# Kernel tuning notes

Measured on AMD Instinct MI355X. Metric: run time of the kernel, lower is better.

The kernel has to match this reference:

```python
import jax, jax.numpy as jnp
import numpy as np

DIM = 512
DEPTH = 6
HEADS = 8
DH = 64
WS = 256
INNER = HEADS * DH  # 512
FF_INNER = int(DIM * 4 * 2 / 3)  # 1365
QK_SCALE = 8.0


def l2norm(x):
    n = jnp.linalg.norm(x, axis=-1, keepdims=True)
    return x / jnp.maximum(n, 1e-12)


def rotate_half(x):
    x1, x2 = jnp.split(x, 2, axis=-1)
    return jnp.concatenate([-x2, x1], axis=-1)


def apply_xpos_rotary(q, k, n, dh, scale_base):
    # SinusoidalEmbeddings with use_xpos=True, scale_base = window_size // 2
    inv_freq = 1.0 / (10000.0 ** (jnp.arange(0, dh, 2, dtype=jnp.float32) / dh))  # (dh/2,)
    t = jnp.arange(n, dtype=jnp.float32)
    freqs = t[:, None] * inv_freq[None, :]                     # (n, dh/2)
    freqs = jnp.concatenate([freqs, freqs], axis=-1)           # (n, dh)
    sv = (jnp.arange(0, dh, 2, dtype=jnp.float32) + 0.4 * dh) / (1.4 * dh)  # (dh/2,)
    power = (t - n // 2) / scale_base
    xs = sv[None, :] ** power[:, None]                         # (n, dh/2)
    xs = jnp.concatenate([xs, xs], axis=-1)                    # (n, dh)
    cos, sin = jnp.cos(freqs), jnp.sin(freqs)
    q = q * cos * xs + rotate_half(q) * sin * xs
    k = k * cos / xs + rotate_half(k) * sin / xs
    return q, k


def local_mha(x, Wqkv, Wo, q_scale, k_scale):
    b, n, d = x.shape
    qkv = x @ Wqkv                                             # (b, n, 3*INNER)
    q, k, v = jnp.split(qkv, 3, axis=-1)
    to_heads = lambda t: t.reshape(b, n, HEADS, DH).transpose(0, 2, 1, 3)
    q, k, v = to_heads(q), to_heads(k), to_heads(v)            # (b, h, n, dh)
    # qk rmsnorm (l2 norm + learned per-dim scale), fixed attn scale = 8
    q = l2norm(q) * q_scale
    k = l2norm(k) * k_scale
    q, k = apply_xpos_rotary(q, k, n, DH, WS // 2)
    w = n // WS
    bucket = lambda t: t.reshape(b, HEADS, w, WS, DH)
    bq, bk, bv = bucket(q), bucket(k), bucket(v)
    # look_around: prepend previous window (look_backward=1, look_forward=0)
    def look_around(t):
        prev = jnp.concatenate([jnp.zeros_like(t[:, :, :1]), t[:, :, :-1]], axis=2)
        return jnp.concatenate([prev, t], axis=3)              # (b, h, w, 2*WS, dh)
    bk2, bv2 = look_around(bk), look_around(bv)
    # positions and masks (causal + exact windowsize + pad)
    tq = jnp.arange(n, dtype=jnp.int32).reshape(w, WS)
    tk_prev = jnp.concatenate([jnp.full((1, WS), -1, dtype=jnp.int32), tq[:-1]], axis=0)
    tk = jnp.concatenate([tk_prev, tq], axis=1)                # (w, 2*WS)
    diff = tq[:, :, None] - tk[:, None, :]
    allowed = (diff >= 0) & (diff <= WS) & (tk[:, None, :] >= 0)  # (w, WS, 2*WS)
    sim = jnp.einsum('bhwie,bhwje->bhwij', bq, bk2) * QK_SCALE
    sim = jnp.where(allowed, sim, -jnp.finfo(sim.dtype).max)
    attn = jax.nn.softmax(sim, axis=-1)
    o = jnp.einsum('bhwij,bhwje->bhwie', attn, bv2)            # (b, h, w, WS, dh)
    o = o.reshape(b, HEADS, n, DH).transpose(0, 2, 1, 3).reshape(b, n, INNER)
    return o @ Wo


def feedforward(x, W1, b1, W2, b2):
    h = x @ W1 + b1
    a, g = jnp.split(h, 2, axis=-1)
    return (a * jax.nn.gelu(g, approximate=False)) @ W2 + b2


def setup_inputs() -> dict:
    key = jax.random.key(0)
    ks = jax.random.split(key, 8)
    s = 0.02
    x = jax.random.normal(ks[0], (1, 8192, DIM), dtype=jnp.float32)
    Wqkv = jax.random.normal(ks[1], (DEPTH, DIM, 3 * INNER), dtype=jnp.float32) * s
    Wo = jax.random.normal(ks[2], (DEPTH, INNER, DIM), dtype=jnp.float32) * s
    q_scale = jnp.ones((DEPTH, DH), dtype=jnp.float32)
    k_scale = jnp.ones((DEPTH, DH), dtype=jnp.float32)
    W1 = jax.random.normal(ks[3], (DEPTH, DIM, 2 * FF_INNER), dtype=jnp.float32) * s
    b1 = jnp.zeros((DEPTH, 2 * FF_INNER), dtype=jnp.float32)
    W2 = jax.random.normal(ks[4], (DEPTH, FF_INNER, DIM), dtype=jnp.float32) * s
    b2 = jnp.zeros((DEPTH, DIM), dtype=jnp.float32)
    return {"x": x, "Wqkv": Wqkv, "Wo": Wo, "q_scale": q_scale, "k_scale": k_scale,
            "W1": W1, "b1": b1, "W2": W2, "b2": b2}


def reference(x, Wqkv, Wo, q_scale, k_scale, W1, b1, W2, b2):
    for i in range(DEPTH):
        x = local_mha(x, Wqkv[i], Wo[i], q_scale[i], k_scale[i]) + x
        x = feedforward(x, W1[i], b1[i], W2[i], b2[i]) + x
    return x
```

## Files before the change

### kernel.cpp

```cpp
#include <hip/hip_runtime.h>
#include <hip/hip_bf16.h>
#include <math.h>

typedef short s16x8 __attribute__((ext_vector_type(8)));
typedef short s16x4 __attribute__((ext_vector_type(4)));
typedef float f32x4 __attribute__((ext_vector_type(4)));

#define MFMA(A,B,C) __builtin_amdgcn_mfma_f32_16x16x32_bf16((A),(B),(C),0,0,0)

typedef __attribute__((address_space(3))) unsigned int lds_u32;
typedef __attribute__((address_space(1))) const unsigned int glb_u32;
__device__ __forceinline__ void gload16(const short* g, const short* l){
  __builtin_amdgcn_global_load_lds((glb_u32*)g, (lds_u32*)l, 16, 0, 0);
}

__device__ __forceinline__ float bf2f(short u){
  unsigned int x = ((unsigned int)(unsigned short)u) << 16;
  return __builtin_bit_cast(float, x);
}
__device__ __forceinline__ short f2bf(float f){
  unsigned int x = __builtin_bit_cast(unsigned int, f);
  x += 0x7fffu + ((x >> 16) & 1u);
  return (short)(x >> 16);
}
__device__ __forceinline__ float gelu_t(float x){
  float u = x + 0.044715f*x*x*x;
  float e = __expf(1.5957691216057308f*u);
  float th = 1.f - 2.f/(e + 1.f);
  return 0.5f*x*(1.f + th);
}

__device__ __forceinline__ void xcd_swz(int gx, int gy, int &bx, int &by){
  int id = bx + by*gx;
  int nwg = gx*gy;
  int q = nwg >> 3, r = nwg & 7;
  int xcd = id & 7, idx = id >> 3;
  int nid = (xcd < r ? xcd*(q+1) : r*(q+1) + (xcd-r)*q) + idx;
  bx = nid % gx; by = nid / gx;
}

#define FFI 1365
#define FFIP 1376

template<int HAS_BIAS, int HAS_RES, int OUT_F32, int OUT_BF16>
__global__ __launch_bounds__(512) void gemm_k(
    const short* __restrict__ A, const short* __restrict__ Bt,
    const float* __restrict__ bias, const float* __restrict__ res,
    float* __restrict__ outF, short* __restrict__ outB,
    int M, int N, int K)
{
  __shared__ short As[2][128*32];
  __shared__ short Bs[2][128*32];
  const int tid = threadIdx.x;
  const int lane = tid & 63, wv = tid >> 6;
  const int g = lane >> 4, qi = lane & 15;
  int bx = blockIdx.x, by = blockIdx.y;
  xcd_swz(gridDim.x, gridDim.y, bx, by);
  const int m0 = bx * 128, n0 = by * 128;
  const int wm = (wv >> 2) * 64, wn = (wv & 3) * 32;

  const int sr = tid >> 2, sc = (tid & 3) * 8;
  const short* Ag = A  + (size_t)(m0 + sr)*K + sc;
  const short* Bg = Bt + (size_t)(n0 + sr)*K + sc;

  f32x4 acc[4][2];
  #pragma unroll
  for (int i=0;i<4;i++)
    #pragma unroll
    for (int j=0;j<2;j++) acc[i][j] = (f32x4){0.f,0.f,0.f,0.f};

  auto stage = [&](int buf, int k0){
    gload16(Ag + k0, &As[buf][wv*512]);
    gload16(Bg + k0, &Bs[buf][wv*512]);
  };

  const int nt = K >> 5;
  stage(0, 0);
  __syncthreads();
  for (int t = 0; t < nt; ++t) {
    const int cur = t & 1;
    if (t + 1 < nt) stage(cur ^ 1, (t+1) << 5);
    s16x8 af[4], bf[2];
    #pragma unroll
    for (int mi=0;mi<4;mi++) af[mi] = *(const s16x8*)&As[cur][(wm+mi*16+qi)*32 + g*8];
    #pragma unroll
    for (int ni=0;ni<2;ni++) bf[ni] = *(const s16x8*)&Bs[cur][(wn+ni*16+qi)*32 + g*8];
    #pragma unroll
    for (int mi=0;mi<4;mi++)
      #pragma unroll
      for (int ni=0;ni<2;ni++)
        acc[mi][ni] = MFMA(af[mi], bf[ni], acc[mi][ni]);
    __syncthreads();
  }
  #pragma unroll
  for (int mi=0;mi<4;mi++){
    #pragma unroll
    for (int r=0;r<4;r++){
      int row = m0 + wm + mi*16 + g*4 + r;
      #pragma unroll
      for (int ni=0;ni<2;ni++){
        int col = n0 + wn + ni*16 + qi;
        float v = acc[mi][ni][r];
        if (HAS_BIAS) v += bias[col];
        if (HAS_RES)  v += res[(size_t)row*N + col];
        if (OUT_F32)  outF[(size_t)row*N + col] = v;
        if (OUT_BF16) outB[(size_t)row*N + col] = f2bf(v);
      }
    }
  }
}

template<int HAS_BIAS, int HAS_RES, int OUT_F32, int OUT_BF16>
__global__ __launch_bounds__(256) void gemm64_k(
    const short* __restrict__ A, const short* __restrict__ Bt,
    const float* __restrict__ bias, const float* __restrict__ res,
    float* __restrict__ outF, short* __restrict__ outB,
    int M, int N, int K)
{
  __shared__ short As[2][64*32];
  __shared__ short Bs[2][64*32];
  const int tid = threadIdx.x;
  const int lane = tid & 63, wv = tid >> 6;
  const int g = lane >> 4, qi = lane & 15;
  int bx = blockIdx.x, by = blockIdx.y;
  xcd_swz(gridDim.x, gridDim.y, bx, by);
  const int m0 = bx * 64, n0 = by * 64;
  const int wm = (wv >> 1) * 32, wn = (wv & 1) * 32;

  const int sr = tid >> 2, sc = (tid & 3) * 8;
  const short* Ag = A  + (size_t)(m0 + sr)*K + sc;
  const short* Bg = Bt + (size_t)(n0 + sr)*K + sc;

  f32x4 acc[2][2];
  #pragma unroll
  for (int i=0;i<2;i++)
    #pragma unroll
    for (int j=0;j<2;j++) acc[i][j] = (f32x4){0.f,0.f,0.f,0.f};

  auto stage = [&](int buf, int k0){
    gload16(Ag + k0, &As[buf][wv*512]);
    gload16(Bg + k0, &Bs[buf][wv*512]);
  };

  const int nt = K >> 5;
  stage(0, 0);
  __syncthreads();
  for (int t = 0; t < nt; ++t) {
    const int cur = t & 1;
    if (t + 1 < nt) stage(cur ^ 1, (t+1) << 5);
    s16x8 af[2], bf[2];
    #pragma unroll
    for (int mi=0;mi<2;mi++) af[mi] = *(const s16x8*)&As[cur][(wm+mi*16+qi)*32 + g*8];
    #pragma unroll
    for (int ni=0;ni<2;ni++) bf[ni] = *(const s16x8*)&Bs[cur][(wn+ni*16+qi)*32 + g*8];
    #pragma unroll
    for (int mi=0;mi<2;mi++)
      #pragma unroll
      for (int ni=0;ni<2;ni++)
        acc[mi][ni] = MFMA(af[mi], bf[ni], acc[mi][ni]);
    __syncthreads();
  }
  #pragma unroll
  for (int mi=0;mi<2;mi++){
    #pragma unroll
    for (int r=0;r<4;r++){
      int row = m0 + wm + mi*16 + g*4 + r;
      #pragma unroll
      for (int ni=0;ni<2;ni++){
        int col = n0 + wn + ni*16 + qi;
        float v = acc[mi][ni][r];
        if (HAS_BIAS) v += bias[col];
        if (HAS_RES)  v += res[(size_t)row*N + col];
        if (OUT_F32)  outF[(size_t)row*N + col] = v;
        if (OUT_BF16) outB[(size_t)row*N + col] = f2bf(v);
      }
    }
  }
}

__global__ __launch_bounds__(512) void geglu_k(
    const short* __restrict__ A, const short* __restrict__ Bt,
    const float* __restrict__ b1, short* __restrict__ hg)
{
  __shared__ short As[2][128*32];
  __shared__ short Ba[2][128*32];
  __shared__ short Bg[2][128*32];
  const int tid = threadIdx.x;
  const int lane = tid & 63, wv = tid >> 6;
  const int g = lane >> 4, qi = lane & 15;
  int bx = blockIdx.x, by = blockIdx.y;
  xcd_swz(gridDim.x, gridDim.y, bx, by);
  const int m0 = bx * 128, n0 = by * 128;
  const int wm = (wv >> 2) * 64, wn = (wv & 3) * 32;

  const int sr = tid >> 2, sc = (tid & 3) * 8;
  const short* Ag = A + (size_t)(m0 + sr)*512 + sc;
  const short* Pa = Bt + (size_t)min(n0 + sr, FFI-1)*512 + sc;
  const short* Pg = Bt + (size_t)min(FFI + n0 + sr, 2729)*512 + sc;

  f32x4 aa[4][2], ag[4][2];
  #pragma unroll
  for (int i=0;i<4;i++)
    #pragma unroll
    for (int j=0;j<2;j++){ aa[i][j]=(f32x4){0.f,0.f,0.f,0.f}; ag[i][j]=(f32x4){0.f,0.f,0.f,0.f}; }

  auto stage = [&](int buf, int k0){
    gload16(Ag + k0, &As[buf][wv*512]);
    gload16(Pa + k0, &Ba[buf][wv*512]);
    gload16(Pg + k0, &Bg[buf][wv*512]);
  };

  stage(0, 0);
  __syncthreads();
  for (int t = 0; t < 16; ++t) {
    const int cur = t & 1;
    if (t + 1 < 16) stage(cur ^ 1, (t+1) << 5);
    s16x8 af[4], bfa[2], bfg[2];
    #pragma unroll
    for (int mi=0;mi<4;mi++) af[mi] = *(const s16x8*)&As[cur][(wm+mi*16+qi)*32 + g*8];
    #pragma unroll
    for (int ni=0;ni<2;ni++){ bfa[ni] = *(const s16x8*)&Ba[cur][(wn+ni*16+qi)*32 + g*8];
                              bfg[ni] = *(const s16x8*)&Bg[cur][(wn+ni*16+qi)*32 + g*8]; }
    #pragma unroll
    for (int mi=0;mi<4;mi++)
      #pragma unroll
      for (int ni=0;ni<2;ni++){
        aa[mi][ni] = MFMA(af[mi], bfa[ni], aa[mi][ni]);
        ag[mi][ni] = MFMA(af[mi], bfg[ni], ag[mi][ni]);
      }
    __syncthreads();
  }
  #pragma unroll
  for (int mi=0;mi<4;mi++){
    #pragma unroll
    for (int r=0;r<4;r++){
      int row = m0 + wm + mi*16 + g*4 + r;
      #pragma unroll
      for (int ni=0;ni<2;ni++){
        int col = n0 + wn + ni*16 + qi;
        if (col < FFI){
          float va = aa[mi][ni][r] + b1[col];
          float vg = ag[mi][ni][r] + b1[FFI+col];
          hg[(size_t)row*FFIP + col] = f2bf(va * gelu_t(vg));
        } else if (col < FFIP){
          hg[(size_t)row*FFIP + col] = 0;
        }
      }
    }
  }
}

__global__ void rope_k(float* __restrict__ tab){
  int n = blockIdx.x, dd = threadIdx.x;
  int i = dd & 31;
  double invf = pow(10000.0, -(double)i/32.0);
  double fr = (double)n * invf;
  double c = cos(fr), s = sin(fr);
  double sv = (2.0*i + 25.6)/89.6;
  double pw = ((double)n - 4096.0)/128.0;
  double xs = pow(sv, pw);
  size_t o = (size_t)n*64 + dd;
  tab[o]            = (float)(c*xs);
  tab[524288+o]     = (float)(s*xs);
  tab[2*524288+o]   = (float)(c/xs);
  tab[3*524288+o]   = (float)(s/xs);
}

__global__ __launch_bounds__(256) void wtrans_k(
    const float* __restrict__ src, short* __restrict__ dst,
    int K, int N, int Kp, long srcStride, long dstStride)
{
  __shared__ float t[64][65];
  const float* s = src + (size_t)blockIdx.z * srcStride;
  short* d = dst + (size_t)blockIdx.z * dstStride;
  int n0 = blockIdx.x*64, k0 = blockIdx.y*64;
  int tid = threadIdx.x;
  #pragma unroll
  for (int p=0;p<4;p++){
    int task = p*256+tid;
    int r = task>>4, c = (task&15)*4;
    int k = k0 + r;
    #pragma unroll
    for (int e=0;e<4;e++){
      int n = n0+c+e;
      t[r][c+e] = (k<K && n<N) ? s[(size_t)k*N+n] : 0.f;
    }
  }
  __syncthreads();
  #pragma unroll
  for (int p=0;p<2;p++){
    int task = p*256+tid;
    int nr = task>>3, kg=(task&7)*8;
    int n = n0+nr;
    if (n < N && (k0+kg) < Kp){
      s16x8 v;
      #pragma unroll
      for (int j=0;j<8;j++) v[j] = f2bf(t[kg+j][nr]);
      *(s16x8*)(d + (size_t)n*Kp + k0 + kg) = v;
    }
  }
}

__global__ void cast_k(const float* __restrict__ in, short* __restrict__ out){
  int i = (blockIdx.x*256+threadIdx.x)*4;
  float4 v = *(const float4*)(in+i);
  s16x4 o = { f2bf(v.x), f2bf(v.y), f2bf(v.z), f2bf(v.w) };
  *(s16x4*)(out+i) = o;
}

__global__ __launch_bounds__(256) void qkprep_k(
    const short* __restrict__ qkv, const float* __restrict__ tab,
    const float* __restrict__ qs, const float* __restrict__ ks,
    short* __restrict__ qrot, short* __restrict__ krot)
{
  int wv = threadIdx.x >> 6, lane = threadIdx.x & 63;
  float qsc = qs[lane], ksc = ks[lane];
  #pragma unroll
  for (int it=0; it<8; ++it){
    int wid = it*8192 + blockIdx.x*4 + wv;
    int n = wid >> 3, h = wid & 7;
    float qv = bf2f(qkv[(size_t)n*1536 + h*64 + lane]);
    float kv = bf2f(qkv[(size_t)n*1536 + 512 + h*64 + lane]);
    float sq = qv*qv, sk = kv*kv;
    #pragma unroll
    for (int m=1;m<64;m<<=1){ sq += __shfl_xor(sq,m,64); sk += __shfl_xor(sk,m,64); }
    qv *= qsc / fmaxf(sqrtf(sq), 1e-12f);
    kv *= ksc / fmaxf(sqrtf(sk), 1e-12f);
    float qo = __shfl_xor(qv,32,64), ko = __shfl_xor(kv,32,64);
    float sgn = (lane<32)? -1.f : 1.f;
    size_t to = (size_t)n*64 + lane;
    float cq = tab[to], sxq = tab[524288+to], ck = tab[2*524288+to], sxk = tab[3*524288+to];
    qrot[((size_t)h*8192+n)*64+lane] = f2bf(qv*cq + sgn*qo*sxq);
    krot[((size_t)h*8192+n)*64+lane] = f2bf(kv*ck + sgn*ko*sxk);
  }
}

__global__ __launch_bounds__(256) void vtrans_k(const short* __restrict__ qkv, short* __restrict__ vt){
  __shared__ short t[64][72];
  int n0 = blockIdx.x*64, h = blockIdx.y;
  int tid = threadIdx.x;
  #pragma unroll
  for (int p=0;p<2;p++){
    int task = p*256+tid;
    int r = task>>3, cg = (task&7)*8;
    *(s16x8*)&t[r][cg] = *(const s16x8*)(qkv + (size_t)(n0+r)*1536 + 1024 + h*64 + cg);
  }
  __syncthreads();
  #pragma unroll
  for (int p=0;p<2;p++){
    int task = p*256+tid;
    int d = task>>3, nb = (task&7)*8;
    s16x8 v;
    #pragma unroll
    for (int j=0;j<8;j++) v[j] = t[nb+j][d];
    *(s16x8*)(vt + ((size_t)h*64+d)*8192 + n0 + nb) = v;
  }
}

__global__ __launch_bounds__(512,1) void attn_k(
    const short* __restrict__ qrot, const short* __restrict__ krot,
    const short* __restrict__ vt, short* __restrict__ attn_o)
{
  __shared__ short Ks[128][72];
  __shared__ short Vs[64][136];
  const int bxx = blockIdx.x, h = blockIdx.y;
  const int w = bxx >> 1, half = bxx & 1;
  const int tid = threadIdx.x, lane = tid & 63, wv = tid >> 6;
  const int g = lane >> 4, qi = lane & 15;
  const int wq = half*128 + wv*16;
  const int q0abs = w*256 + wq;
  s16x8 qf[2];
  {
    const short* p = qrot + ((size_t)h*8192 + q0abs + qi)*64 + g*8;
    qf[0] = *(const s16x8*)p;
    qf[1] = *(const s16x8*)(p + 32);
  }
  f32x4 oacc[4];
  #pragma unroll
  for (int j=0;j<4;j++) oacc[j]=(f32x4){0.f,0.f,0.f,0.f};
  float mrun = -1e30f, lrun = 0.f;
  const int kvbase = w*256 - 256;
  for (int s=half; s<half+3; ++s){
    __syncthreads();
    #pragma unroll
    for (int p=0;p<2;p++){
      int task = p*512 + tid;
      {
        int r = task>>3, cg = (task&7)*8;
        int jg = kvbase + s*128 + r;
        s16x8 v = {0,0,0,0,0,0,0,0};
        if (jg>=0) v = *(const s16x8*)(krot + ((size_t)h*8192+jg)*64 + cg);
        *(s16x8*)&Ks[r][cg] = v;
      }
      {
        int dd = task>>4, cg = (task&15)*8;
        int jg = kvbase + s*128 + cg;
        s16x8 v = {0,0,0,0,0,0,0,0};
        if (jg>=0) v = *(const s16x8*)(vt + ((size_t)h*64+dd)*8192 + jg);
        *(s16x8*)&Vs[dd][cg] = v;
      }
    }
    __syncthreads();
    for (int cc=0;cc<2;cc++){
      const int jlo = s*128 + cc*64;
      if (jlo + 63 < wq) continue;
      if (jlo > wq + 271) continue;
      if (w==0 && jlo < 256) continue;
      f32x4 sacc[4];
      #pragma unroll
      for (int i=0;i<4;i++) sacc[i]=(f32x4){0.f,0.f,0.f,0.f};
      #pragma unroll
      for (int ks=0;ks<2;ks++){
        s16x8 kf[4];
        #pragma unroll
        for (int mi=0;mi<4;mi++) kf[mi] = *(const s16x8*)&Ks[cc*64+mi*16+qi][ks*32+g*8];
        #pragma unroll
        for (int mi=0;mi<4;mi++)
          sacc[mi] = MFMA(kf[mi], qf[ks], sacc[mi]);
      }
      const bool interior = (jlo >= wq+15) && (jlo+63 <= wq+256);
      float cmax = -1e30f;
      #pragma unroll
      for (int mi=0;mi<4;mi++)
        #pragma unroll
        for (int r=0;r<4;r++){
          float x = sacc[mi][r] * 8.f;
          if (!interior){
            int j = jlo + mi*16 + g*4 + r;
            int ql = wq + qi;
            if (j < ql || j > ql+256) x = -1e30f;
          }
          sacc[mi][r] = x;
          cmax = fmaxf(cmax, x);
        }
      cmax = fmaxf(cmax, __shfl_xor(cmax,16,64));
      cmax = fmaxf(cmax, __shfl_xor(cmax,32,64));
      float mn = fmaxf(mrun, cmax);
      float scl = __expf(mrun - mn);
      mrun = mn;
      float ps = 0.f;
      s16x8 pf[2];
      #pragma unroll
      for (int t=0;t<2;t++)
        #pragma unroll
        for (int hh=0; hh<2; hh++){
          int mi = 2*t+hh;
          #pragma unroll
          for (int r=0;r<4;r++){
            float pv = __expf(sacc[mi][r]-mn);
            ps += pv;
            pf[t][hh*4+r] = f2bf(pv);
          }
        }
      ps += __shfl_xor(ps,16,64);
      ps += __shfl_xor(ps,32,64);
      lrun = lrun*scl + ps;
      #pragma unroll
      for (int mi=0;mi<4;mi++) oacc[mi] *= scl;
      #pragma unroll
      for (int t=0;t<2;t++)
        #pragma unroll
        for (int mi=0;mi<4;mi++){
          const short* vp = &Vs[mi*16+qi][cc*64 + t*32 + g*4];
          s16x4 lo = *(const s16x4*)vp;
          s16x4 hi = *(const s16x4*)(vp+16);
          s16x8 vf = {lo[0],lo[1],lo[2],lo[3],hi[0],hi[1],hi[2],hi[3]};
          oacc[mi] = MFMA(vf, pf[t], oacc[mi]);
        }
    }
  }
  float inv = 1.f / lrun;
  #pragma unroll
  for (int mi=0;mi<4;mi++){
    s16x4 st;
    #pragma unroll
    for (int r=0;r<4;r++) st[r] = f2bf(oacc[mi][r]*inv);
    *(s16x4*)(attn_o + (size_t)(q0abs+qi)*512 + h*64 + mi*16 + g*4) = st;
  }
}

extern "C" void kernel_launch(void* const* d_in, const int* in_sizes, int n_in,
                              void* d_out, int out_size, void* d_ws, size_t ws_size,
                              hipStream_t stream)
{
  const float* x_in = (const float*)d_in[0];
  const float* Wqkv = (const float*)d_in[1];
  const float* Wo   = (const float*)d_in[2];
  const float* qsc  = (const float*)d_in[3];
  const float* ksc  = (const float*)d_in[4];
  const float* W1   = (const float*)d_in[5];
  const float* b1   = (const float*)d_in[6];
  const float* W2   = (const float*)d_in[7];
  const float* b2   = (const float*)d_in[8];
  float* xf = (float*)d_out;

  char* ws = (char*)d_ws;
  size_t off = 0;
  float* tab  = (float*)(ws + off); off += (size_t)4*8192*64*4;
  short* WqkvT= (short*)(ws + off); off += (size_t)6*1536*512*2;
  short* WoT  = (short*)(ws + off); off += (size_t)6*512*512*2;
  short* W1T  = (short*)(ws + off); off += (size_t)6*2730*512*2;
  short* W2T  = (short*)(ws + off); off += (size_t)6*512*1376*2;
  short* xbf  = (short*)(ws + off); off += (size_t)8192*512*2;
  short* qkv  = (short*)(ws + off); off += (size_t)8192*1536*2;
  short* qrot = (short*)(ws + off); off += (size_t)8*8192*64*2;
  short* krot = (short*)(ws + off); off += (size_t)8*8192*64*2;
  short* vt   = (short*)(ws + off); off += (size_t)8*8192*64*2;
  short* attno= (short*)(ws + off); off += (size_t)8192*512*2;
  short* hg   = (short*)(ws + off); off += (size_t)8192*1376*2;

  hipMemcpyAsync(xf, x_in, (size_t)8192*512*4, hipMemcpyDeviceToDevice, stream);
  rope_k<<<8192, 64, 0, stream>>>(tab);
  wtrans_k<<<dim3(24,8,6),256,0,stream>>>(Wqkv, WqkvT, 512,1536,512, (long)512*1536, (long)1536*512);
  wtrans_k<<<dim3(8,8,6),256,0,stream>>>(Wo, WoT, 512,512,512, (long)512*512,(long)512*512);
  wtrans_k<<<dim3(43,8,6),256,0,stream>>>(W1, W1T, 512,2730,512, (long)512*2730,(long)2730*512);
  wtrans_k<<<dim3(8,22,6),256,0,stream>>>(W2, W2T, 1365,512,1376, (long)1365*512,(long)512*1376);
  cast_k<<<4096,256,0,stream>>>(x_in, xbf);

  for (int l=0;l<6;l++){
    gemm_k<0,0,0,1><<<dim3(64,12),512,0,stream>>>(xbf, WqkvT + (size_t)l*1536*512,
        nullptr, nullptr, nullptr, qkv, 8192,1536,512);
    qkprep_k<<<2048,256,0,stream>>>(qkv, tab, qsc + l*64, ksc + l*64, qrot, krot);
    vtrans_k<<<dim3(128,8),256,0,stream>>>(qkv, vt);
    attn_k<<<dim3(64,8),512,0,stream>>>(qrot, krot, vt, attno);
    gemm64_k<0,1,1,1><<<dim3(128,8),256,0,stream>>>(attno, WoT + (size_t)l*512*512,
        nullptr, xf, xf, xbf, 8192,512,512);
    geglu_k<<<dim3(64,11),512,0,stream>>>(xbf, W1T + (size_t)l*2730*512, b1 + (size_t)l*2730, hg);
    gemm64_k<1,1,1,1><<<dim3(128,8),256,0,stream>>>(hg, W2T + (size_t)l*512*1376,
        b2 + (size_t)l*512, xf, xf, xbf, 8192,512,1376);
  }
}
```

Before: 1.146 ms.

## Fuse QK norm, rotary and V transpose into QKV GEMM epilogue; retile output GEMMs

The QKV projection GEMM now does the per-head L2 norm, learned scale and xpos rotary in its epilogue, and writes the transposed V directly. This removes the bf16 qkv intermediate and the separate qkprep and vtrans kernels. The Wo and W2 GEMMs move from 64x64 to 128x64 tiles to get more reuse per block. The rotary table is now built with float intrinsics instead of double precision, which adds a small accuracy risk and extra LDS passes and barriers in the fused epilogue.

```diff
diff --git a/kernel.cpp b/kernel.cpp
--- a/kernel.cpp
+++ b/kernel.cpp
@@ -42,15 +42,14 @@
 #define FFI 1365
 #define FFIP 1376
 
-template<int HAS_BIAS, int HAS_RES, int OUT_F32, int OUT_BF16>
-__global__ __launch_bounds__(512) void gemm_k(
+__global__ __launch_bounds__(512) void qkv_fused_k(
     const short* __restrict__ A, const short* __restrict__ Bt,
-    const float* __restrict__ bias, const float* __restrict__ res,
-    float* __restrict__ outF, short* __restrict__ outB,
-    int M, int N, int K)
+    const float* __restrict__ tab,
+    const float* __restrict__ qs, const float* __restrict__ ksc_,
+    short* __restrict__ qrot, short* __restrict__ krot, short* __restrict__ vt)
 {
-  __shared__ short As[2][128*32];
-  __shared__ short Bs[2][128*32];
+  __shared__ short SBUF[16896];
+  __shared__ float ss[2][128][2];
   const int tid = threadIdx.x;
   const int lane = tid & 63, wv = tid >> 6;
   const int g = lane >> 4, qi = lane & 15;
@@ -60,6 +59,137 @@
   const int wm = (wv >> 2) * 64, wn = (wv & 3) * 32;
 
   const int sr = tid >> 2, sc = (tid & 3) * 8;
+  const short* Ag = A  + (size_t)(m0 + sr)*512 + sc;
+  const short* Bg = Bt + (size_t)(n0 + sr)*512 + sc;
+
+  f32x4 acc[4][2];
+  #pragma unroll
+  for (int i=0;i<4;i++)
+    #pragma unroll
+    for (int j=0;j<2;j++) acc[i][j] = (f32x4){0.f,0.f,0.f,0.f};
+
+  auto stage = [&](int buf, int k0){
+    gload16(Ag + k0, SBUF + buf*4096 + wv*512);
+    gload16(Bg + k0, SBUF + 8192 + buf*4096 + wv*512);
+  };
+
+  stage(0, 0);
+  __syncthreads();
+  for (int t = 0; t < 16; ++t) {
+    const int cur = t & 1;
+    if (t + 1 < 16) stage(cur ^ 1, (t+1) << 5);
+    s16x8 af[4], bf[2];
+    #pragma unroll
+    for (int mi=0;mi<4;mi++) af[mi] = *(const s16x8*)&SBUF[cur*4096 + (wm+mi*16+qi)*32 + g*8];
+    #pragma unroll
+    for (int ni=0;ni<2;ni++) bf[ni] = *(const s16x8*)&SBUF[8192 + cur*4096 + (wn+ni*16+qi)*32 + g*8];
+    #pragma unroll
+    for (int mi=0;mi<4;mi++)
+      #pragma unroll
+      for (int ni=0;ni<2;ni++)
+        acc[mi][ni] = MFMA(af[mi], bf[ni], acc[mi][ni]);
+    __syncthreads();
+  }
+  const int hl = (wv & 3) >> 1;
+  if (by < 8) {
+    const bool isq = (by < 4);
+    const int head = (isq ? by : (by-4))*2 + hl;
+    const float* scale = isq ? qs : ksc_;
+    #pragma unroll
+    for (int mi=0;mi<4;mi++)
+      #pragma unroll
+      for (int r=0;r<4;r++){
+        float s = acc[mi][0][r]*acc[mi][0][r] + acc[mi][1][r]*acc[mi][1][r];
+        s += __shfl_xor(s,1,64); s += __shfl_xor(s,2,64);
+        s += __shfl_xor(s,4,64); s += __shfl_xor(s,8,64);
+        if (qi == 0) ss[wv & 1][wm + mi*16 + g*4 + r][hl] = s;
+      }
+    float sc0 = scale[(wn + qi) & 63], sc1 = scale[(wn + 16 + qi) & 63];
+    __syncthreads();
+    float nva[4][2][4];
+    #pragma unroll
+    for (int mi=0;mi<4;mi++)
+      #pragma unroll
+      for (int r=0;r<4;r++){
+        int rowl = wm + mi*16 + g*4 + r;
+        float stot = ss[0][rowl][hl] + ss[1][rowl][hl];
+        float inv = 1.f / fmaxf(sqrtf(stot), 1e-12f);
+        #pragma unroll
+        for (int ni=0;ni<2;ni++){
+          float nv = acc[mi][ni][r] * (ni ? sc1 : sc0) * inv;
+          nva[mi][ni][r] = nv;
+          int col = wn + ni*16 + qi;
+          SBUF[rowl*132 + col] = f2bf(nv);
+        }
+      }
+    __syncthreads();
+    short* outp = isq ? qrot : krot;
+    const float* tc = tab + (isq ? 0 : 2*524288);
+    const float* ts = tab + (isq ? 524288 : 3*524288);
+    #pragma unroll
+    for (int mi=0;mi<4;mi++)
+      #pragma unroll
+      for (int r=0;r<4;r++){
+        int rowl = wm + mi*16 + g*4 + r;
+        int n = m0 + rowl;
+        #pragma unroll
+        for (int ni=0;ni<2;ni++){
+          int col = wn + ni*16 + qi;
+          int d = col & 63;
+          float partner = bf2f(SBUF[rowl*132 + (col ^ 32)]);
+          float sgn = (d < 32) ? -1.f : 1.f;
+          size_t to = (size_t)n*64 + d;
+          float out = nva[mi][ni][r]*tc[to] + sgn*partner*ts[to];
+          outp[((size_t)head*8192 + n)*64 + d] = f2bf(out);
+        }
+      }
+  } else {
+    const int hbase = (by - 8) * 2;
+    #pragma unroll
+    for (int mi=0;mi<4;mi++)
+      #pragma unroll
+      for (int r=0;r<4;r++){
+        int rowl = wm + mi*16 + g*4 + r;
+        #pragma unroll
+        for (int ni=0;ni<2;ni++){
+          int col = wn + ni*16 + qi;
+          SBUF[rowl*132 + col] = f2bf(acc[mi][ni][r]);
+        }
+      }
+    __syncthreads();
+    #pragma unroll
+    for (int p=0;p<4;p++){
+      int task = p*512 + tid;
+      int hl2 = task >> 10;
+      int d = (task >> 4) & 63;
+      int nb = (task & 15) * 8;
+      int col = hl2*64 + d;
+      s16x8 v;
+      #pragma unroll
+      for (int j=0;j<8;j++) v[j] = SBUF[(nb+j)*132 + col];
+      *(s16x8*)(vt + ((size_t)(hbase+hl2)*64 + d)*8192 + m0 + nb) = v;
+    }
+  }
+}
+
+template<int HAS_BIAS, int HAS_RES, int OUT_F32, int OUT_BF16>
+__global__ __launch_bounds__(256) void gemm128x64_k(
+    const short* __restrict__ A, const short* __restrict__ Bt,
+    const float* __restrict__ bias, const float* __restrict__ res,
+    float* __restrict__ outF, short* __restrict__ outB,
+    int M, int N, int K)
+{
+  __shared__ short As[2][128*32];
+  __shared__ short Bs[2][64*32];
+  const int tid = threadIdx.x;
+  const int lane = tid & 63, wv = tid >> 6;
+  const int g = lane >> 4, qi = lane & 15;
+  int bx = blockIdx.x, by = blockIdx.y;
+  xcd_swz(gridDim.x, gridDim.y, bx, by);
+  const int m0 = bx * 128, n0 = by * 64;
+  const int wm = (wv >> 1) * 64, wn = (wv & 1) * 32;
+
+  const int sr = wv*16 + (lane >> 2), sc = (lane & 3) * 8;
   const short* Ag = A  + (size_t)(m0 + sr)*K + sc;
   const short* Bg = Bt + (size_t)(n0 + sr)*K + sc;
 
@@ -71,6 +201,7 @@
 
   auto stage = [&](int buf, int k0){
     gload16(Ag + k0, &As[buf][wv*512]);
+    gload16(Ag + (size_t)64*K + k0, &As[buf][2048 + wv*512]);
     gload16(Bg + k0, &Bs[buf][wv*512]);
   };
 
@@ -94,74 +225,6 @@
   }
   #pragma unroll
   for (int mi=0;mi<4;mi++){
-    #pragma unroll
-    for (int r=0;r<4;r++){
-      int row = m0 + wm + mi*16 + g*4 + r;
-      #pragma unroll
-      for (int ni=0;ni<2;ni++){
-        int col = n0 + wn + ni*16 + qi;
-        float v = acc[mi][ni][r];
-        if (HAS_BIAS) v += bias[col];
-        if (HAS_RES)  v += res[(size_t)row*N + col];
-        if (OUT_F32)  outF[(size_t)row*N + col] = v;
-        if (OUT_BF16) outB[(size_t)row*N + col] = f2bf(v);
-      }
-    }
-  }
-}
-
-template<int HAS_BIAS, int HAS_RES, int OUT_F32, int OUT_BF16>
-__global__ __launch_bounds__(256) void gemm64_k(
-    const short* __restrict__ A, const short* __restrict__ Bt,
-    const float* __restrict__ bias, const float* __restrict__ res,
-    float* __restrict__ outF, short* __restrict__ outB,
-    int M, int N, int K)
-{
-  __shared__ short As[2][64*32];
-  __shared__ short Bs[2][64*32];
-  const int tid = threadIdx.x;
-  const int lane = tid & 63, wv = tid >> 6;
-  const int g = lane >> 4, qi = lane & 15;
-  int bx = blockIdx.x, by = blockIdx.y;
-  xcd_swz(gridDim.x, gridDim.y, bx, by);
-  const int m0 = bx * 64, n0 = by * 64;
-  const int wm = (wv >> 1) * 32, wn = (wv & 1) * 32;
-
-  const int sr = tid >> 2, sc = (tid & 3) * 8;
-  const short* Ag = A  + (size_t)(m0 + sr)*K + sc;
-  const short* Bg = Bt + (size_t)(n0 + sr)*K + sc;
-
-  f32x4 acc[2][2];
-  #pragma unroll
-  for (int i=0;i<2;i++)
-    #pragma unroll
-    for (int j=0;j<2;j++) acc[i][j] = (f32x4){0.f,0.f,0.f,0.f};
-
-  auto stage = [&](int buf, int k0){
-    gload16(Ag + k0, &As[buf][wv*512]);
-    gload16(Bg + k0, &Bs[buf][wv*512]);
-  };
-
-  const int nt = K >> 5;
-  stage(0, 0);
-  __syncthreads();
-  for (int t = 0; t < nt; ++t) {
-    const int cur = t & 1;
-    if (t + 1 < nt) stage(cur ^ 1, (t+1) << 5);
-    s16x8 af[2], bf[2];
-    #pragma unroll
-    for (int mi=0;mi<2;mi++) af[mi] = *(const s16x8*)&As[cur][(wm+mi*16+qi)*32 + g*8];
-    #pragma unroll
-    for (int ni=0;ni<2;ni++) bf[ni] = *(const s16x8*)&Bs[cur][(wn+ni*16+qi)*32 + g*8];
-    #pragma unroll
-    for (int mi=0;mi<2;mi++)
-      #pragma unroll
-      for (int ni=0;ni<2;ni++)
-        acc[mi][ni] = MFMA(af[mi], bf[ni], acc[mi][ni]);
-    __syncthreads();
-  }
-  #pragma unroll
-  for (int mi=0;mi<2;mi++){
     #pragma unroll
     for (int r=0;r<4;r++){
       int row = m0 + wm + mi*16 + g*4 + r;
@@ -253,17 +316,17 @@
 __global__ void rope_k(float* __restrict__ tab){
   int n = blockIdx.x, dd = threadIdx.x;
   int i = dd & 31;
-  double invf = pow(10000.0, -(double)i/32.0);
-  double fr = (double)n * invf;
-  double c = cos(fr), s = sin(fr);
-  double sv = (2.0*i + 25.6)/89.6;
-  double pw = ((double)n - 4096.0)/128.0;
-  double xs = pow(sv, pw);
+  float invf = exp2f(-(float)i * (13.287712379549449f/32.0f));
+  float fr = (float)n * invf;
+  float c = cosf(fr), s = sinf(fr);
+  float sv = (2.0f*i + 25.6f)/89.6f;
+  float pw = ((float)n - 4096.0f)/128.0f;
+  float xs = exp2f(pw * log2f(sv));
   size_t o = (size_t)n*64 + dd;
-  tab[o]            = (float)(c*xs);
-  tab[524288+o]     = (float)(s*xs);
-  tab[2*524288+o]   = (float)(c/xs);
-  tab[3*524288+o]   = (float)(s/xs);
+  tab[o]            = c*xs;
+  tab[524288+o]     = s*xs;
+  tab[2*524288+o]   = c/xs;
+  tab[3*524288+o]   = s/xs;
 }
 
 __global__ __launch_bounds__(256) void wtrans_k(
@@ -306,55 +369,6 @@
   float4 v = *(const float4*)(in+i);
   s16x4 o = { f2bf(v.x), f2bf(v.y), f2bf(v.z), f2bf(v.w) };
   *(s16x4*)(out+i) = o;
-}
-
-__global__ __launch_bounds__(256) void qkprep_k(
-    const short* __restrict__ qkv, const float* __restrict__ tab,
-    const float* __restrict__ qs, const float* __restrict__ ks,
-    short* __restrict__ qrot, short* __restrict__ krot)
-{
-  int wv = threadIdx.x >> 6, lane = threadIdx.x & 63;
-  float qsc = qs[lane], ksc = ks[lane];
-  #pragma unroll
-  for (int it=0; it<8; ++it){
-    int wid = it*8192 + blockIdx.x*4 + wv;
-    int n = wid >> 3, h = wid & 7;
-    float qv = bf2f(qkv[(size_t)n*1536 + h*64 + lane]);
-    float kv = bf2f(qkv[(size_t)n*1536 + 512 + h*64 + lane]);
-    float sq = qv*qv, sk = kv*kv;
-    #pragma unroll
-    for (int m=1;m<64;m<<=1){ sq += __shfl_xor(sq,m,64); sk += __shfl_xor(sk,m,64); }
-    qv *= qsc / fmaxf(sqrtf(sq), 1e-12f);
-    kv *= ksc / fmaxf(sqrtf(sk), 1e-12f);
-    float qo = __shfl_xor(qv,32,64), ko = __shfl_xor(kv,32,64);
-    float sgn = (lane<32)? -1.f : 1.f;
-    size_t to = (size_t)n*64 + lane;
-    float cq = tab[to], sxq = tab[524288+to], ck = tab[2*524288+to], sxk = tab[3*524288+to];
-    qrot[((size_t)h*8192+n)*64+lane] = f2bf(qv*cq + sgn*qo*sxq);
-    krot[((size_t)h*8192+n)*64+lane] = f2bf(kv*ck + sgn*ko*sxk);
-  }
-}
-
-__global__ __launch_bounds__(256) void vtrans_k(const short* __restrict__ qkv, short* __restrict__ vt){
-  __shared__ short t[64][72];
-  int n0 = blockIdx.x*64, h = blockIdx.y;
-  int tid = threadIdx.x;
-  #pragma unroll
-  for (int p=0;p<2;p++){
-    int task = p*256+tid;
-    int r = task>>3, cg = (task&7)*8;
-    *(s16x8*)&t[r][cg] = *(const s16x8*)(qkv + (size_t)(n0+r)*1536 + 1024 + h*64 + cg);
-  }
-  __syncthreads();
-  #pragma unroll
-  for (int p=0;p<2;p++){
-    int task = p*256+tid;
-    int d = task>>3, nb = (task&7)*8;
-    s16x8 v;
-    #pragma unroll
-    for (int j=0;j<8;j++) v[j] = t[nb+j][d];
-    *(s16x8*)(vt + ((size_t)h*64+d)*8192 + n0 + nb) = v;
-  }
 }
 
 __global__ __launch_bounds__(512,1) void attn_k(
@@ -502,7 +516,6 @@
   short* W1T  = (short*)(ws + off); off += (size_t)6*2730*512*2;
   short* W2T  = (short*)(ws + off); off += (size_t)6*512*1376*2;
   short* xbf  = (short*)(ws + off); off += (size_t)8192*512*2;
-  short* qkv  = (short*)(ws + off); off += (size_t)8192*1536*2;
   short* qrot = (short*)(ws + off); off += (size_t)8*8192*64*2;
   short* krot = (short*)(ws + off); off += (size_t)8*8192*64*2;
   short* vt   = (short*)(ws + off); off += (size_t)8*8192*64*2;
@@ -518,15 +531,13 @@
   cast_k<<<4096,256,0,stream>>>(x_in, xbf);
 
   for (int l=0;l<6;l++){
-    gemm_k<0,0,0,1><<<dim3(64,12),512,0,stream>>>(xbf, WqkvT + (size_t)l*1536*512,
-        nullptr, nullptr, nullptr, qkv, 8192,1536,512);
-    qkprep_k<<<2048,256,0,stream>>>(qkv, tab, qsc + l*64, ksc + l*64, qrot, krot);
-    vtrans_k<<<dim3(128,8),256,0,stream>>>(qkv, vt);
+    qkv_fused_k<<<dim3(64,12),512,0,stream>>>(xbf, WqkvT + (size_t)l*1536*512,
+        tab, qsc + l*64, ksc + l*64, qrot, krot, vt);
     attn_k<<<dim3(64,8),512,0,stream>>>(qrot, krot, vt, attno);
-    gemm64_k<0,1,1,1><<<dim3(128,8),256,0,stream>>>(attno, WoT + (size_t)l*512*512,
+    gemm128x64_k<0,1,1,1><<<dim3(64,8),256,0,stream>>>(attno, WoT + (size_t)l*512*512,
         nullptr, xf, xf, xbf, 8192,512,512);
     geglu_k<<<dim3(64,11),512,0,stream>>>(xbf, W1T + (size_t)l*2730*512, b1 + (size_t)l*2730, hg);
-    gemm64_k<1,1,1,1><<<dim3(128,8),256,0,stream>>>(hg, W2T + (size_t)l*512*1376,
+    gemm128x64_k<1,1,1,1><<<dim3(64,8),256,0,stream>>>(hg, W2T + (size_t)l*512*1376,
         b2 + (size_t)l*512, xf, xf, xbf, 8192,512,1376);
   }
 }
```

Result: faster. 1.099 ms (-4.1%).
